# Kernel tuning notes

Measured on AMD Instinct MI355X. Metric: run time of the kernel, lower is better.

The kernel has to match this reference:

```python
import jax, jax.numpy as jnp
import numpy as np

TOP_K = 2
ROUTE_SCALE = 1.0


def setup_inputs() -> dict:
    key = jax.random.key(0)
    ks = jax.random.split(key, 8)
    B, S, D = 4, 2048, 2048
    E, I = 8, 1408
    SI = 2 * I  # shared experts inter dim (n_shared_experts * moe_inter_dim)
    s = lambda d: 1.0 / np.sqrt(d)
    return {
        "x": jax.random.normal(ks[0], (B, S, D), jnp.float32),
        "gate_w": jax.random.normal(ks[1], (E, D), jnp.float32) * s(D),
        "w1": jax.random.normal(ks[2], (E, I, D), jnp.float32) * s(D),
        "w2": jax.random.normal(ks[3], (E, D, I), jnp.float32) * s(I),
        "w3": jax.random.normal(ks[4], (E, I, D), jnp.float32) * s(D),
        "sw1": jax.random.normal(ks[5], (SI, D), jnp.float32) * s(D),
        "sw2": jax.random.normal(ks[6], (D, SI), jnp.float32) * s(SI),
        "sw3": jax.random.normal(ks[7], (SI, D), jnp.float32) * s(D),
    }


def reference(x, gate_w, w1, w2, w3, sw1, sw2, sw3):
    B, S, D = x.shape
    E = gate_w.shape[0]
    xt = x.reshape(-1, D)                       # [T, D]
    T = xt.shape[0]

    # Gate: softmax scores in fp32, top-k routing; n_groups=1, no bias,
    # score_func='softmax' -> weights are the top-k softmax probs * route_scale.
    scores = jax.nn.softmax((xt @ gate_w.T).astype(jnp.float32), axis=-1)  # [T, E]
    top_w, top_idx = jax.lax.top_k(scores, TOP_K)
    top_w = (top_w * ROUTE_SCALE).astype(x.dtype)  # [T, K]

    # Dense per-expert combine weights (zero for unrouted experts).
    dense_w = jnp.zeros((T, E), x.dtype).at[jnp.arange(T)[:, None], top_idx].add(top_w)

    # Routed SwiGLU experts: y_t = sum_e dense_w[t,e] * Expert_e(x_t)
    y = jnp.zeros_like(xt)
    for e in range(E):
        h = jax.nn.silu(xt @ w1[e].T) * (xt @ w3[e].T)  # [T, I]
        y = y + dense_w[:, e:e + 1] * (h @ w2[e].T)

    # Shared experts (single SwiGLU MLP over all tokens).
    z = (jax.nn.silu(xt @ sw1.T) * (xt @ sw3.T)) @ sw2.T

    return (y + z).reshape(B, S, D)
```

## Files before the change

### kernel.cpp

```cpp
#include <hip/hip_runtime.h>

#define T_TOK 8192
#define DDIM  2048
#define NEXP  8
#define IDIM  1408
#define SIDIM 2816
#define MAXSLOTS 17408

typedef short  v8s  __attribute__((ext_vector_type(8)));
typedef __bf16 v8bf __attribute__((ext_vector_type(8)));
typedef float  v4f  __attribute__((ext_vector_type(4)));

__device__ __forceinline__ unsigned short f2bf_bits(float f){
  union { float fv; unsigned u; } v; v.fv = f;
  unsigned r = v.u + 0x7fffu + ((v.u >> 16) & 1u);
  return (unsigned short)(r >> 16);
}

__device__ __forceinline__ void gld16(const void* g, void* l){
  __builtin_amdgcn_global_load_lds(
      (const __attribute__((address_space(1))) unsigned int*)g,
      (__attribute__((address_space(3))) unsigned int*)l, 16, 0, 0);
}

__device__ __forceinline__ v4f mfma16(v8s a, v8s b, v4f c){
  return __builtin_amdgcn_mfma_f32_16x16x32_bf16(
      __builtin_bit_cast(v8bf, a), __builtin_bit_cast(v8bf, b), c, 0, 0, 0);
}


__global__ __launch_bounds__(256) void route_init_k(int* rows, float* roww, int* counts){
  int i = blockIdx.x*256 + threadIdx.x;
  if (i < MAXSLOTS){ rows[i] = 0; roww[i] = 0.f; }
  if (i < NEXP) counts[i] = 0;
}

__global__ __launch_bounds__(256) void cvt_bf16_k(const float4* __restrict__ s,
                                                  ushort4* __restrict__ d, int n4){
  int i = blockIdx.x*256 + threadIdx.x;
  int stride = gridDim.x*256;
  for (; i < n4; i += stride){
    float4 v = s[i];
    d[i] = make_ushort4(f2bf_bits(v.x), f2bf_bits(v.y), f2bf_bits(v.z), f2bf_bits(v.w));
  }
}

__global__ __launch_bounds__(256) void gate_cast_k(const float* __restrict__ x,
    const float* __restrict__ gw, unsigned short* __restrict__ xbf,
    int* __restrict__ tidx, float* __restrict__ tw, int* __restrict__ counts){
  int t = threadIdx.x, w = t>>6, lane = t&63;
  int token = blockIdx.x*4 + w;
  const float* xr = x + (size_t)token*DDIM;
  float acc[NEXP];
  #pragma unroll
  for (int e=0;e<NEXP;++e) acc[e]=0.f;
  #pragma unroll
  for (int i=0;i<8;++i){
    int d = i*256 + lane*4;
    float4 xv = *(const float4*)(xr + d);
    *(ushort4*)(xbf + (size_t)token*DDIM + d) =
        make_ushort4(f2bf_bits(xv.x), f2bf_bits(xv.y), f2bf_bits(xv.z), f2bf_bits(xv.w));
    #pragma unroll
    for (int e=0;e<NEXP;++e){
      float4 g = *(const float4*)(gw + e*DDIM + d);
      acc[e] += xv.x*g.x + xv.y*g.y + xv.z*g.z + xv.w*g.w;
    }
  }
  #pragma unroll
  for (int off=32; off; off>>=1){
    #pragma unroll
    for (int e=0;e<NEXP;++e) acc[e] += __shfl_xor(acc[e], off);
  }
  if (lane == 0){
    float mx = acc[0];
    #pragma unroll
    for (int e=1;e<NEXP;++e) mx = fmaxf(mx, acc[e]);
    float p[NEXP], s = 0.f;
    #pragma unroll
    for (int e=0;e<NEXP;++e){ p[e] = __expf(acc[e]-mx); s += p[e]; }
    float inv = 1.f/s;
    #pragma unroll
    for (int e=0;e<NEXP;++e) p[e] *= inv;
    int i0 = 0;
    #pragma unroll
    for (int e=1;e<NEXP;++e) if (p[e] > p[i0]) i0 = e;
    int i1 = (i0==0) ? 1 : 0;
    #pragma unroll
    for (int e=0;e<NEXP;++e) if (e!=i0 && e!=i1 && p[e] > p[i1]) i1 = e;
    tidx[token*2+0] = i0; tidx[token*2+1] = i1;
    tw[token*2+0] = p[i0]; tw[token*2+1] = p[i1];
    atomicAdd(&counts[i0], 1); atomicAdd(&counts[i1], 1);
  }
}

__global__ void route_offsets_k(const int* counts, int* pad_off, int* pad_cnt, int* fill){
  if (threadIdx.x == 0){
    int o = 0;
    for (int e=0;e<NEXP;++e){
      pad_off[e] = o;
      int pc = (counts[e] + 127) & ~127;
      pad_cnt[e] = pc;
      o += pc;
    }
  }
  if (threadIdx.x < NEXP) fill[threadIdx.x] = 0;
}

__global__ __launch_bounds__(256) void scatter_k(const int* __restrict__ tidx,
    const float* __restrict__ tw, const int* __restrict__ pad_off,
    int* __restrict__ fill, int* __restrict__ rows, float* __restrict__ roww){
  int t = blockIdx.x*256 + threadIdx.x;
  int lane = threadIdx.x & 63;
  #pragma unroll
  for (int k=0;k<2;++k){
    int e = tidx[t*2+k];
    float wgt = tw[t*2+k];
    for (int ee=0; ee<NEXP; ++ee){
      unsigned long long m = __ballot(e == ee);
      if (m){
        int leader = __ffsll((unsigned long long)m) - 1;
        int base = 0;
        if (lane == leader) base = atomicAdd(&fill[ee], __popcll(m));
        base = __shfl(base, leader);
        if (e == ee){
          int rank = __popcll(m & ((1ull<<lane)-1ull));
          int pos = pad_off[ee] + base + rank;
          rows[pos] = t; roww[pos] = wgt;
        }
      }
    }
  }
}


template<bool GATHER>
__global__ __launch_bounds__(256,2) void gemm_dual_silu_k(
    const unsigned short* __restrict__ Abase,
    const unsigned short* __restrict__ B0base,
    const unsigned short* __restrict__ B1base,
    unsigned short* __restrict__ Hbase,
    const int* __restrict__ rows,
    const int* __restrict__ pad_off, const int* __restrict__ pad_cnt,
    int K, int N)
{
  int e = blockIdx.z;
  int off = 0, mcnt = T_TOK;
  if (GATHER){ off = pad_off[e]; mcnt = pad_cnt[e]; }
  int brow = blockIdx.x * 128;
  if (brow >= mcnt) return;
  int bcol = blockIdx.y * 128;

  const unsigned short* B0 = B0base + (size_t)e * (size_t)N * (size_t)K;
  const unsigned short* B1 = B1base + (size_t)e * (size_t)N * (size_t)K;
  unsigned short* H = Hbase + (size_t)off * (size_t)N;

  __shared__ unsigned short As [128*32];
  __shared__ unsigned short Bs0[128*32];
  __shared__ unsigned short Bs1[128*32];

  int t = threadIdx.x, w = t>>6, lane = t&63;
  int srow = lane>>2, scol = (lane&3)*8;

  const unsigned short *ag[2], *b0g[2], *b1g[2];
  #pragma unroll
  for (int j=0;j<2;++j){
    int r = brow + j*64 + w*16 + srow;
    int tok = GATHER ? rows[off + r] : r;
    ag[j] = Abase + (size_t)tok*(size_t)K + scol;
    int rb = bcol + j*64 + w*16 + srow;
    b0g[j] = B0 + (size_t)rb*(size_t)K + scol;
    b1g[j] = B1 + (size_t)rb*(size_t)K + scol;
  }

  v4f acc0[4][4], acc1[4][4];
  #pragma unroll
  for (int m=0;m<4;++m)
    #pragma unroll
    for (int n=0;n<4;++n){
      acc0[m][n] = (v4f){0.f,0.f,0.f,0.f};
      acc1[m][n] = (v4f){0.f,0.f,0.f,0.f};
    }

  int fr = lane & 15, fq = lane >> 4;
  int wr = (w>>1)*64, wc = (w&1)*64;

  for (int k0=0; k0<K; k0+=32){
    __syncthreads();
    #pragma unroll
    for (int j=0;j<2;++j){
      int lo = (j*256 + w*64)*16;
      gld16(ag[j]  + k0, (char*)As  + lo);
      gld16(b0g[j] + k0, (char*)Bs0 + lo);
      gld16(b1g[j] + k0, (char*)Bs1 + lo);
    }
    __syncthreads();
    v8s af[4];
    #pragma unroll
    for (int m=0;m<4;++m) af[m] = *(const v8s*)(As + (wr + m*16 + fr)*32 + fq*8);
    #pragma unroll
    for (int n=0;n<4;++n){
      v8s b0f = *(const v8s*)(Bs0 + (wc + n*16 + fr)*32 + fq*8);
      v8s b1f = *(const v8s*)(Bs1 + (wc + n*16 + fr)*32 + fq*8);
      #pragma unroll
      for (int m=0;m<4;++m){
        acc0[m][n] = mfma16(af[m], b0f, acc0[m][n]);
        acc1[m][n] = mfma16(af[m], b1f, acc1[m][n]);
      }
    }
  }

  #pragma unroll
  for (int m=0;m<4;++m){
    #pragma unroll
    for (int n=0;n<4;++n){
      #pragma unroll
      for (int r=0;r<4;++r){
        int row = brow + wr + m*16 + fq*4 + r;
        int col = bcol + wc + n*16 + fr;
        float a = acc0[m][n][r];
        float b = acc1[m][n][r];
        float h = a * b / (1.f + __expf(-a));
        H[(size_t)row*(size_t)N + col] = f2bf_bits(h);
      }
    }
  }
}

template<bool ATOMIC>
__global__ __launch_bounds__(256,2) void gemm_out_k(
    const unsigned short* __restrict__ Abase,
    const unsigned short* __restrict__ Bbase,
    float* __restrict__ out,
    const int* __restrict__ rows, const float* __restrict__ roww,
    const int* __restrict__ pad_off, const int* __restrict__ pad_cnt,
    int K)
{
  int e = blockIdx.z;
  int off = 0, mcnt = T_TOK;
  if (ATOMIC){ off = pad_off[e]; mcnt = pad_cnt[e]; }
  int brow = blockIdx.x * 128;
  if (brow >= mcnt) return;
  int bcol = blockIdx.y * 128;

  const unsigned short* A  = Abase + (size_t)off * (size_t)K;
  const unsigned short* Bm = Bbase + (size_t)e * (size_t)DDIM * (size_t)K;

  __shared__ unsigned short As[128*32];
  __shared__ unsigned short Bs[128*32];

  int t = threadIdx.x, w = t>>6, lane = t&63;
  int srow = lane>>2, scol = (lane&3)*8;

  const unsigned short *ag[2], *bg[2];
  #pragma unroll
  for (int j=0;j<2;++j){
    ag[j] = A  + (size_t)(brow + j*64 + w*16 + srow)*(size_t)K + scol;
    bg[j] = Bm + (size_t)(bcol + j*64 + w*16 + srow)*(size_t)K + scol;
  }

  v4f acc[4][4];
  #pragma unroll
  for (int m=0;m<4;++m)
    #pragma unroll
    for (int n=0;n<4;++n) acc[m][n] = (v4f){0.f,0.f,0.f,0.f};

  int fr = lane & 15, fq = lane >> 4;
  int wr = (w>>1)*64, wc = (w&1)*64;

  for (int k0=0; k0<K; k0+=32){
    __syncthreads();
    #pragma unroll
    for (int j=0;j<2;++j){
      int lo = (j*256 + w*64)*16;
      gld16(ag[j] + k0, (char*)As + lo);
      gld16(bg[j] + k0, (char*)Bs + lo);
    }
    __syncthreads();
    v8s af[4];
    #pragma unroll
    for (int m=0;m<4;++m) af[m] = *(const v8s*)(As + (wr + m*16 + fr)*32 + fq*8);
    #pragma unroll
    for (int n=0;n<4;++n){
      v8s bf = *(const v8s*)(Bs + (wc + n*16 + fr)*32 + fq*8);
      #pragma unroll
      for (int m=0;m<4;++m) acc[m][n] = mfma16(af[m], bf, acc[m][n]);
    }
  }

  #pragma unroll
  for (int m=0;m<4;++m){
    #pragma unroll
    for (int r=0;r<4;++r){
      int slot = brow + wr + m*16 + fq*4 + r;
      int tok = slot; float wgt = 1.f;
      if (ATOMIC){ tok = rows[off+slot]; wgt = roww[off+slot]; }
      #pragma unroll
      for (int n=0;n<4;++n){
        int col = bcol + wc + n*16 + fr;
        float v = acc[m][n][r];
        if (ATOMIC) atomicAdd(out + (size_t)tok*DDIM + col, wgt*v);
        else        out[(size_t)slot*DDIM + col] = v;
      }
    }
  }
}


extern "C" void kernel_launch(void* const* d_in, const int* in_sizes, int n_in,
                              void* d_out, int out_size, void* d_ws, size_t ws_size,
                              hipStream_t stream)
{
  const float* x   = (const float*)d_in[0];
  const float* gw  = (const float*)d_in[1];
  const float* w1  = (const float*)d_in[2];
  const float* w2  = (const float*)d_in[3];
  const float* w3  = (const float*)d_in[4];
  const float* sw1 = (const float*)d_in[5];
  const float* sw2 = (const float*)d_in[6];
  const float* sw3 = (const float*)d_in[7];
  float* out = (float*)d_out;

  char* p = (char*)d_ws;
  auto alloc = [&](size_t bytes)->char*{
    char* r = p; p += (bytes + 255) & ~(size_t)255; return r;
  };
  const size_t NW  = (size_t)NEXP*IDIM*DDIM;
  const size_t NSW = (size_t)SIDIM*DDIM;

  unsigned short* xbf  = (unsigned short*)alloc((size_t)T_TOK*DDIM*2);
  unsigned short* w1b  = (unsigned short*)alloc(NW*2);
  unsigned short* w3b  = (unsigned short*)alloc(NW*2);
  unsigned short* w2b  = (unsigned short*)alloc(NW*2);
  unsigned short* sw1b = (unsigned short*)alloc(NSW*2);
  unsigned short* sw3b = (unsigned short*)alloc(NSW*2);
  unsigned short* sw2b = (unsigned short*)alloc(NSW*2);
  unsigned short* Hbuf = (unsigned short*)alloc((size_t)MAXSLOTS*IDIM*2);
  int*   tidx    = (int*)  alloc((size_t)T_TOK*2*4);
  float* tw      = (float*)alloc((size_t)T_TOK*2*4);
  int*   rows    = (int*)  alloc((size_t)MAXSLOTS*4);
  float* roww    = (float*)alloc((size_t)MAXSLOTS*4);
  int*   counts  = (int*)  alloc(NEXP*4);
  int*   pad_off = (int*)  alloc(NEXP*4);
  int*   pad_cnt = (int*)  alloc(NEXP*4);
  int*   fill    = (int*)  alloc(NEXP*4);

  route_init_k<<<(MAXSLOTS+255)/256, 256, 0, stream>>>(rows, roww, counts);

  cvt_bf16_k<<<2048, 256, 0, stream>>>((const float4*)w1,  (ushort4*)w1b,  (int)(NW/4));
  cvt_bf16_k<<<2048, 256, 0, stream>>>((const float4*)w3,  (ushort4*)w3b,  (int)(NW/4));
  cvt_bf16_k<<<2048, 256, 0, stream>>>((const float4*)w2,  (ushort4*)w2b,  (int)(NW/4));
  cvt_bf16_k<<<1024, 256, 0, stream>>>((const float4*)sw1, (ushort4*)sw1b, (int)(NSW/4));
  cvt_bf16_k<<<1024, 256, 0, stream>>>((const float4*)sw3, (ushort4*)sw3b, (int)(NSW/4));
  cvt_bf16_k<<<1024, 256, 0, stream>>>((const float4*)sw2, (ushort4*)sw2b, (int)(NSW/4));

  gate_cast_k<<<T_TOK/4, 256, 0, stream>>>(x, gw, xbf, tidx, tw, counts);

  route_offsets_k<<<1, 64, 0, stream>>>(counts, pad_off, pad_cnt, fill);
  scatter_k<<<T_TOK/256, 256, 0, stream>>>(tidx, tw, pad_off, fill, rows, roww);

  gemm_dual_silu_k<false><<<dim3(T_TOK/128, SIDIM/128, 1), 256, 0, stream>>>(
      xbf, sw1b, sw3b, Hbuf, nullptr, nullptr, nullptr, DDIM, SIDIM);
  gemm_out_k<false><<<dim3(T_TOK/128, DDIM/128, 1), 256, 0, stream>>>(
      Hbuf, sw2b, out, nullptr, nullptr, nullptr, nullptr, SIDIM);

  gemm_dual_silu_k<true><<<dim3(T_TOK/128, IDIM/128, NEXP), 256, 0, stream>>>(
      xbf, w1b, w3b, Hbuf, rows, pad_off, pad_cnt, DDIM, IDIM);
  gemm_out_k<true><<<dim3(T_TOK/128, DDIM/128, NEXP), 256, 0, stream>>>(
      Hbuf, w2b, out, rows, roww, pad_off, pad_cnt, IDIM);
}
```

Measured before the change: 1.393 ms.

## Double-buffer LDS tiles and add XCD-aware grouped rasterization to GEMMs

New measurement: 1.970 ms. 41.4% more time.

```diff
diff --git a/kernel.cpp b/kernel.cpp
--- a/kernel.cpp
+++ b/kernel.cpp
@@ -26,6 +26,21 @@
 __device__ __forceinline__ v4f mfma16(v8s a, v8s b, v4f c){
   return __builtin_amdgcn_mfma_f32_16x16x32_bf16(
       __builtin_bit_cast(v8bf, a), __builtin_bit_cast(v8bf, b), c, 0, 0, 0);
+}
+
+__device__ __forceinline__ int2 raster(int bid, int nx, int ny){
+  int nwg = nx * ny;
+  int xcd = bid & 7;
+  int q = nwg >> 3, r = nwg & 7;
+  int lid = (xcd < r ? xcd*(q+1) : r*(q+1) + (xcd-r)*q) + (bid >> 3);
+  const int G = 8;
+  int band  = lid / (G*ny);
+  int first = band * G;
+  int gsz   = (nx - first) < G ? (nx - first) : G;
+  int rem   = lid - band*G*ny;
+  int pm = first + rem % gsz;
+  int pn = rem / gsz;
+  return make_int2(pm, pn);
 }
 
 
@@ -141,22 +156,23 @@
     unsigned short* __restrict__ Hbase,
     const int* __restrict__ rows,
     const int* __restrict__ pad_off, const int* __restrict__ pad_cnt,
-    int K, int N)
+    int K, int N, int ny)
 {
   int e = blockIdx.z;
   int off = 0, mcnt = T_TOK;
   if (GATHER){ off = pad_off[e]; mcnt = pad_cnt[e]; }
-  int brow = blockIdx.x * 128;
+  int2 pmn = raster(blockIdx.x, T_TOK/128, ny);
+  int brow = pmn.x * 128;
   if (brow >= mcnt) return;
-  int bcol = blockIdx.y * 128;
+  int bcol = pmn.y * 128;
 
   const unsigned short* B0 = B0base + (size_t)e * (size_t)N * (size_t)K;
   const unsigned short* B1 = B1base + (size_t)e * (size_t)N * (size_t)K;
   unsigned short* H = Hbase + (size_t)off * (size_t)N;
 
-  __shared__ unsigned short As [128*32];
-  __shared__ unsigned short Bs0[128*32];
-  __shared__ unsigned short Bs1[128*32];
+  __shared__ unsigned short As [2][128*32];
+  __shared__ unsigned short Bs0[2][128*32];
+  __shared__ unsigned short Bs1[2][128*32];
 
   int t = threadIdx.x, w = t>>6, lane = t&63;
   int srow = lane>>2, scol = (lane&3)*8;
@@ -164,8 +180,8 @@
   const unsigned short *ag[2], *b0g[2], *b1g[2];
   #pragma unroll
   for (int j=0;j<2;++j){
-    int r = brow + j*64 + w*16 + srow;
-    int tok = GATHER ? rows[off + r] : r;
+    int rr = brow + j*64 + w*16 + srow;
+    int tok = GATHER ? rows[off + rr] : rr;
     ag[j] = Abase + (size_t)tok*(size_t)K + scol;
     int rb = bcol + j*64 + w*16 + srow;
     b0g[j] = B0 + (size_t)rb*(size_t)K + scol;
@@ -183,30 +199,45 @@
 
   int fr = lane & 15, fq = lane >> 4;
   int wr = (w>>1)*64, wc = (w&1)*64;
-
-  for (int k0=0; k0<K; k0+=32){
-    __syncthreads();
-    #pragma unroll
-    for (int j=0;j<2;++j){
-      int lo = (j*256 + w*64)*16;
-      gld16(ag[j]  + k0, (char*)As  + lo);
-      gld16(b0g[j] + k0, (char*)Bs0 + lo);
-      gld16(b1g[j] + k0, (char*)Bs1 + lo);
-    }
-    __syncthreads();
+  int lo = (w*64 + lane)*16;
+
+  #pragma unroll
+  for (int j=0;j<2;++j){
+    gld16(ag[j],  (char*)As [0] + lo + j*4096);
+    gld16(b0g[j], (char*)Bs0[0] + lo + j*4096);
+    gld16(b1g[j], (char*)Bs1[0] + lo + j*4096);
+  }
+  __syncthreads();
+
+  int nst = K/32;
+  for (int s=0; s<nst; ++s){
+    int cur = s & 1, nxt = cur ^ 1;
+    if (s+1 < nst){
+      int k0 = (s+1)*32;
+      #pragma unroll
+      for (int j=0;j<2;++j){
+        gld16(ag[j]  + k0, (char*)As [nxt] + lo + j*4096);
+        gld16(b0g[j] + k0, (char*)Bs0[nxt] + lo + j*4096);
+        gld16(b1g[j] + k0, (char*)Bs1[nxt] + lo + j*4096);
+      }
+    }
+    const unsigned short* Ac  = As [cur];
+    const unsigned short* B0c = Bs0[cur];
+    const unsigned short* B1c = Bs1[cur];
     v8s af[4];
     #pragma unroll
-    for (int m=0;m<4;++m) af[m] = *(const v8s*)(As + (wr + m*16 + fr)*32 + fq*8);
+    for (int m=0;m<4;++m) af[m] = *(const v8s*)(Ac + (wr + m*16 + fr)*32 + fq*8);
     #pragma unroll
     for (int n=0;n<4;++n){
-      v8s b0f = *(const v8s*)(Bs0 + (wc + n*16 + fr)*32 + fq*8);
-      v8s b1f = *(const v8s*)(Bs1 + (wc + n*16 + fr)*32 + fq*8);
+      v8s b0f = *(const v8s*)(B0c + (wc + n*16 + fr)*32 + fq*8);
+      v8s b1f = *(const v8s*)(B1c + (wc + n*16 + fr)*32 + fq*8);
       #pragma unroll
       for (int m=0;m<4;++m){
         acc0[m][n] = mfma16(af[m], b0f, acc0[m][n]);
         acc1[m][n] = mfma16(af[m], b1f, acc1[m][n]);
       }
     }
+    __syncthreads();
   }
 
   #pragma unroll
@@ -238,15 +269,16 @@
   int e = blockIdx.z;
   int off = 0, mcnt = T_TOK;
   if (ATOMIC){ off = pad_off[e]; mcnt = pad_cnt[e]; }
-  int brow = blockIdx.x * 128;
+  int2 pmn = raster(blockIdx.x, T_TOK/128, DDIM/128);
+  int brow = pmn.x * 128;
   if (brow >= mcnt) return;
-  int bcol = blockIdx.y * 128;
+  int bcol = pmn.y * 128;
 
   const unsigned short* A  = Abase + (size_t)off * (size_t)K;
   const unsigned short* Bm = Bbase + (size_t)e * (size_t)DDIM * (size_t)K;
 
-  __shared__ unsigned short As[128*32];
-  __shared__ unsigned short Bs[128*32];
+  __shared__ unsigned short As[2][128*32];
+  __shared__ unsigned short Bs[2][128*32];
 
   int t = threadIdx.x, w = t>>6, lane = t&63;
   int srow = lane>>2, scol = (lane&3)*8;
@@ -266,25 +298,38 @@
 
   int fr = lane & 15, fq = lane >> 4;
   int wr = (w>>1)*64, wc = (w&1)*64;
-
-  for (int k0=0; k0<K; k0+=32){
+  int lo = (w*64 + lane)*16;
+
+  #pragma unroll
+  for (int j=0;j<2;++j){
+    gld16(ag[j], (char*)As[0] + lo + j*4096);
+    gld16(bg[j], (char*)Bs[0] + lo + j*4096);
+  }
+  __syncthreads();
+
+  int nst = K/32;
+  for (int s=0; s<nst; ++s){
+    int cur = s & 1, nxt = cur ^ 1;
+    if (s+1 < nst){
+      int k0 = (s+1)*32;
+      #pragma unroll
+      for (int j=0;j<2;++j){
+        gld16(ag[j] + k0, (char*)As[nxt] + lo + j*4096);
+        gld16(bg[j] + k0, (char*)Bs[nxt] + lo + j*4096);
+      }
+    }
+    const unsigned short* Ac = As[cur];
+    const unsigned short* Bc = Bs[cur];
+    v8s af[4];
+    #pragma unroll
+    for (int m=0;m<4;++m) af[m] = *(const v8s*)(Ac + (wr + m*16 + fr)*32 + fq*8);
+    #pragma unroll
+    for (int n=0;n<4;++n){
+      v8s bf = *(const v8s*)(Bc + (wc + n*16 + fr)*32 + fq*8);
+      #pragma unroll
+      for (int m=0;m<4;++m) acc[m][n] = mfma16(af[m], bf, acc[m][n]);
+    }
     __syncthreads();
-    #pragma unroll
-    for (int j=0;j<2;++j){
-      int lo = (j*256 + w*64)*16;
-      gld16(ag[j] + k0, (char*)As + lo);
-      gld16(bg[j] + k0, (char*)Bs + lo);
-    }
-    __syncthreads();
-    v8s af[4];
-    #pragma unroll
-    for (int m=0;m<4;++m) af[m] = *(const v8s*)(As + (wr + m*16 + fr)*32 + fq*8);
-    #pragma unroll
-    for (int n=0;n<4;++n){
-      v8s bf = *(const v8s*)(Bs + (wc + n*16 + fr)*32 + fq*8);
-      #pragma unroll
-      for (int m=0;m<4;++m) acc[m][n] = mfma16(af[m], bf, acc[m][n]);
-    }
   }
 
   #pragma unroll
@@ -358,13 +403,13 @@
   route_offsets_k<<<1, 64, 0, stream>>>(counts, pad_off, pad_cnt, fill);
   scatter_k<<<T_TOK/256, 256, 0, stream>>>(tidx, tw, pad_off, fill, rows, roww);
 
-  gemm_dual_silu_k<false><<<dim3(T_TOK/128, SIDIM/128, 1), 256, 0, stream>>>(
-      xbf, sw1b, sw3b, Hbuf, nullptr, nullptr, nullptr, DDIM, SIDIM);
-  gemm_out_k<false><<<dim3(T_TOK/128, DDIM/128, 1), 256, 0, stream>>>(
+  gemm_dual_silu_k<false><<<dim3((T_TOK/128)*(SIDIM/128), 1, 1), 256, 0, stream>>>(
+      xbf, sw1b, sw3b, Hbuf, nullptr, nullptr, nullptr, DDIM, SIDIM, SIDIM/128);
+  gemm_out_k<false><<<dim3((T_TOK/128)*(DDIM/128), 1, 1), 256, 0, stream>>>(
       Hbuf, sw2b, out, nullptr, nullptr, nullptr, nullptr, SIDIM);
 
-  gemm_dual_silu_k<true><<<dim3(T_TOK/128, IDIM/128, NEXP), 256, 0, stream>>>(
-      xbf, w1b, w3b, Hbuf, rows, pad_off, pad_cnt, DDIM, IDIM);
-  gemm_out_k<true><<<dim3(T_TOK/128, DDIM/128, NEXP), 256, 0, stream>>>(
+  gemm_dual_silu_k<true><<<dim3((T_TOK/128)*(IDIM/128), 1, NEXP), 256, 0, stream>>>(
+      xbf, w1b, w3b, Hbuf, rows, pad_off, pad_cnt, DDIM, IDIM, IDIM/128);
+  gemm_out_k<true><<<dim3((T_TOK/128)*(DDIM/128), 1, NEXP), 256, 0, stream>>>(
       Hbuf, w2b, out, rows, roww, pad_off, pad_cnt, IDIM);
 }
```
